# Performance work log

Measured on AMD Instinct MI355X. Metric: run time of the kernel, lower is better.

## Reference

```python
import jax, jax.numpy as jnp
import numpy as np
import math

PHI = (1.0 + math.sqrt(5.0)) / 2.0
ALPHA = 0.01
I_ROT = math.pi / 2.0
B, IN, H = 4096, 1024, 1024
GIN = IN + 4 * H  # input + 2H (h flat) + 2H (surfaced flat)


def _mag(z):
    return jnp.sqrt(z[..., 0] ** 2 + z[..., 1] ** 2 + 1e-8)


def _phase(z):
    return jnp.arctan2(z[..., 1], z[..., 0] + 1e-10)


@jax.custom_vjp
def fractal_compress(mag):
    m = jnp.maximum(mag, 1e-8)
    return m ** (2.0 / 3.0)


def _fc_fwd(mag):
    m = jnp.maximum(mag, 1e-8)
    c = m ** (2.0 / 3.0)
    return c, c / (m + 1e-6)


def _fc_bwd(ratio, g):
    return (g * jnp.minimum(ratio, 2.0),)


fractal_compress.defvjp(_fc_fwd, _fc_bwd)


def converge(z):
    mag = _mag(z)
    ph = _phase(z)
    cm = fractal_compress(mag)
    return jnp.stack([cm * jnp.cos(ph), cm * jnp.sin(ph)], axis=-1)


def resonance_gate(a, b):
    d = _phase(a) - _phase(b)
    return jnp.cos(d / 2.0) ** 2


def _uni(k, shape, fan_in):
    s = (1.0 / PHI) / math.sqrt(fan_in)
    return jax.random.uniform(k, shape, jnp.float32, -s, s)


def setup_inputs() -> dict:
    key = jax.random.key(0)
    ks = jax.random.split(key, 12)
    return {
        "x_t": jax.random.normal(ks[0], (B, IN), jnp.float32),
        "h_prev": jax.random.normal(ks[1], (B, H, 2), jnp.float32),
        "c_prev": jax.random.normal(ks[2], (B, H, 2), jnp.float32),
        "d_prev": jax.random.normal(ks[3], (B, H, 2), jnp.float32),
        "b_prev": jax.random.uniform(ks[4], (B, 1), jnp.float32),
        "Wf_w": _uni(ks[5], (H, GIN), GIN), "Wf_b": jnp.zeros((H,), jnp.float32),
        "Wi_w": _uni(ks[6], (H, GIN), GIN), "Wi_b": jnp.zeros((H,), jnp.float32),
        "Wo_w": _uni(ks[7], (H, GIN), GIN), "Wo_b": jnp.zeros((H,), jnp.float32),
        "Wc_w": _uni(ks[8], (2 * H, GIN), GIN), "Wc_b": jnp.zeros((2 * H,), jnp.float32),
        "Wr_w": _uni(ks[9], (2 * H, IN), IN), "Wr_b": jnp.zeros((2 * H,), jnp.float32),
        "theta": jnp.full((H,), I_ROT, jnp.float32),
    }


def reference(x_t, h_prev, c_prev, d_prev, b_prev,
              Wf_w, Wf_b, Wi_w, Wi_b, Wo_w, Wo_b, Wc_w, Wc_b, Wr_w, Wr_b, theta):
    batch = x_t.shape[0]
    hid = theta.shape[0]

    # boundary: real input -> complex
    x_complex = (x_t @ Wr_w.T + Wr_b).reshape(batch, hid, 2)

    # memory surfacing from the (detached) worldline
    d_read = jax.lax.stop_gradient(d_prev)
    T = resonance_gate(x_complex, d_read)                      # (B, H)
    d_mag = _mag(d_read)[..., None]                            # (B, H, 1)
    d_normed = d_read / (d_mag + 1e-8)
    d_scale = jnp.sqrt(jnp.clip(d_mag, 1e-6, 20.0))
    surfaced = d_normed * d_scale * T[..., None]               # (B, H, 2)

    combined = jnp.concatenate(
        [x_t, h_prev.reshape(batch, -1), surfaced.reshape(batch, -1)], axis=-1)

    f_raw = combined @ Wf_w.T + Wf_b
    i_raw = combined @ Wi_w.T + Wi_b
    o_raw = combined @ Wo_w.T + Wo_b

    temperature = (2.0 * b_prev + 1e-4)[..., None]             # (B, 1, 1)
    gate_stack = jnp.stack([f_raw, i_raw, o_raw], axis=-1)     # (B, H, 3)
    gw = jax.nn.softmax(gate_stack / temperature, axis=-1)
    f_t, i_t, o_t = gw[..., 0], gw[..., 1], gw[..., 2]

    g_raw = combined @ Wc_w.T + Wc_b
    g_t = jnp.stack([jnp.tanh(g_raw[:, :hid]), jnp.tanh(g_raw[:, hid:])], axis=-1)

    # convergence: released surface -> fractal-compressed -> worldline
    released = (1.0 - f_t)[..., None] * c_prev
    compressed = jnp.clip(converge(released), -10.0, 10.0)
    d_t = jax.lax.stop_gradient(d_prev) + ALPHA * compressed
    d_mag_new = _mag(d_t)[..., None]
    d_t = jnp.where(d_mag_new > 20.0, d_t * (20.0 / d_mag_new), d_t)

    # cell update + i-rotation
    c_updated = f_t[..., None] * c_prev + i_t[..., None] * g_t
    cos_t = jnp.cos(theta)[None, :, None]
    sin_t = jnp.sin(theta)[None, :, None]
    cr, ci = c_updated[..., 0:1], c_updated[..., 1:2]
    c_t = jnp.concatenate([cos_t * cr - sin_t * ci, sin_t * cr + cos_t * ci], axis=-1)

    c_squashed = jnp.stack([jnp.tanh(c_t[..., 0]), jnp.tanh(c_t[..., 1])], axis=-1)
    h_raw = o_t[..., None] * c_squashed
    G = resonance_gate(h_raw, d_t)
    h_t = G[..., None] * h_raw

    # balance update from energy split
    conv_e = (_mag(released) ** 2).sum(axis=-1, keepdims=True)
    emer_e = (_mag(h_t) ** 2).sum(axis=-1, keepdims=True)
    b_measured = conv_e / (conv_e + emer_e + 1e-8)
    b_t = 0.99 * b_prev + 0.01 * b_measured

    h_t = jnp.nan_to_num(h_t, nan=0.0)
    c_t = jnp.nan_to_num(c_t, nan=0.0)
    d_t = jnp.nan_to_num(d_t, nan=0.0)
    b_t = jnp.nan_to_num(b_t, nan=0.5)
    return (h_t, c_t, d_t, b_t)
```

## Files before the change

### kernel.cpp

```cpp
#include <hip/hip_runtime.h>
#include <math.h>

typedef unsigned short u16;
typedef unsigned int u32;
typedef u16 u16x4 __attribute__((ext_vector_type(4)));
typedef float f32x2 __attribute__((ext_vector_type(2)));
typedef float f32x4 __attribute__((ext_vector_type(4)));
typedef __bf16 bf16x8 __attribute__((ext_vector_type(8)));

#define CAPF 256

__device__ __forceinline__ u16 f2bf(float f){
  u32 u = __builtin_bit_cast(u32, f);
  u32 r = u + 0x7FFFu + ((u >> 16) & 1u);
  return (u16)(r >> 16);
}
__device__ __forceinline__ float bf2f(u16 h){
  u32 u = ((u32)h) << 16;
  return __builtin_bit_cast(float, u);
}
__device__ __forceinline__ float ftanh(float x){
  float e = __expf(2.f*x);
  return 1.f - 2.f/(e+1.f);
}

typedef __attribute__((address_space(1))) const unsigned int gas_u32;
typedef __attribute__((address_space(3))) unsigned int las_u32;
__device__ __forceinline__ void gload_lds16(const void* g, void* l){
  __builtin_amdgcn_global_load_lds((gas_u32*)g, (las_u32*)l, 16, 0, 0);
}

__global__ __launch_bounds__(256) void prep0(
    const float* __restrict__ x, const float* __restrict__ h,
    u16* __restrict__ cA, u16* __restrict__ xlo,
    const float* __restrict__ Wr, u16* __restrict__ Wr_hi, u16* __restrict__ Wr_lo,
    const float* __restrict__ bp, int* __restrict__ idx, int* __restrict__ smap,
    float* __restrict__ rawfix)
{
  const int bx = blockIdx.x, tid = threadIdx.x;
  if (bx < 12288){
    int b = bx / 3, cb = bx - b*3;
    int c0 = (cb*256 + tid)*4;
    f32x4 v;
    if (c0 < 1024) v = *(const f32x4*)(x + (size_t)b*1024 + c0);
    else           v = *(const f32x4*)(h + (size_t)b*2048 + (c0-1024));
    u16x4 hi4;
    #pragma unroll
    for (int j=0;j<4;++j) hi4[j]=f2bf(v[j]);
    *(u16x4*)(cA + (size_t)b*5120 + c0) = hi4;
    if (c0 < 1024){
      u16x4 lo4;
      #pragma unroll
      for (int j=0;j<4;++j) lo4[j]=f2bf(v[j]-bf2f(hi4[j]));
      *(u16x4*)(xlo + (size_t)b*1024 + c0) = lo4;
    }
  } else if (bx < 14336){
    int i = (bx-12288)*256 + tid;
    f32x4 v = *(const f32x4*)(Wr + (size_t)i*4);
    u16x4 oh, ol;
    #pragma unroll
    for (int j=0;j<4;++j){ u16 hh=f2bf(v[j]); oh[j]=hh; ol[j]=f2bf(v[j]-bf2f(hh)); }
    *(u16x4*)(Wr_hi + (size_t)i*4) = oh;
    *(u16x4*)(Wr_lo + (size_t)i*4) = ol;
  } else if (bx < 15104){
    int i = (bx-14336)*256 + tid;
    *(f32x4*)(rawfix + (size_t)i*4) = f32x4{0.f,0.f,0.f,0.f};
  } else {
    __shared__ int cnt;
    if (tid==0) cnt=0;
    __syncthreads();
    for (int i=tid; i<4096; i+=256){
      int p = -1;
      if (bp[i] < 0.04f){
        p = atomicAdd(&cnt,1);
        if (p < CAPF) idx[1+p]=i;
      }
      smap[i] = p;
    }
    __syncthreads();
    if (tid==0) idx[0] = min(cnt, CAPF);
  }
}

__global__ __launch_bounds__(256) void cvtW3(
    const float* __restrict__ W0, const float* __restrict__ W1, const float* __restrict__ W2,
    u16* __restrict__ out)
{
  int i = blockIdx.x*256 + threadIdx.x;
  int seg = i / 1310720;
  int w = i - seg*1310720;
  const float* src = (seg==0) ? W0 : (seg==1 ? W1 : W2);
  f32x4 v = *(const f32x4*)(src + (size_t)w*4);
  u16x4 o;
  #pragma unroll
  for (int j=0;j<4;++j) o[j]=f2bf(v[j]);
  *(u16x4*)(out + (size_t)seg*5242880 + (size_t)w*4) = o;
}

__global__ __launch_bounds__(256) void cvt_hi(const float* __restrict__ in, u16* __restrict__ out, int n4){
  int i = blockIdx.x*256 + threadIdx.x;
  if (i >= n4) return;
  f32x4 v = *(const f32x4*)(in + (size_t)i*4);
  u16x4 o;
  #pragma unroll
  for (int j=0;j<4;++j) o[j]=f2bf(v[j]);
  *(u16x4*)(out + (size_t)i*4) = o;
}

__global__ __launch_bounds__(256) void prep_surf(const float* __restrict__ xc, const float* __restrict__ dp,
                                                 const int* __restrict__ smap, float* __restrict__ Scmp,
                                                 u16* __restrict__ cA){
  int i = blockIdx.x*256 + threadIdx.x;
  int b = i >> 10, h = i & 1023;
  f32x2 z = *(const f32x2*)(xc + 2*(size_t)i);
  f32x2 d = *(const f32x2*)(dp + 2*(size_t)i);
  float zx = z[0] + 1e-10f, dx = d[0] + 1e-10f;
  float hz = sqrtf(zx*zx + z[1]*z[1]);
  float hd = sqrtf(dx*dx + d[1]*d[1]);
  float cosd = (zx*dx + z[1]*d[1]) / fmaxf(hz*hd, 1e-30f);
  float T = 0.5f + 0.5f*cosd;
  float dmag = sqrtf(d[0]*d[0] + d[1]*d[1] + 1e-8f);
  float dscale = sqrtf(fminf(fmaxf(dmag, 1e-6f), 20.0f));
  float s = T * dscale / (dmag + 1e-8f);
  float o0 = d[0]*s, o1 = d[1]*s;
  u32 pk = (u32)f2bf(o0) | ((u32)f2bf(o1) << 16);
  *(u32*)&cA[(size_t)b*5120 + 3072 + 2*h] = pk;
  int p = smap[b];
  if (p >= 0 && p < CAPF)
    *(f32x2*)(Scmp + ((size_t)p*1024 + h)*2) = f32x2{o0, o1};
}

#define STG2B(U, BW) do{ int uc_ = min((U), NH-1); \
    const u16* sa_ = Ah + aS + (size_t)uc_*32; \
    u16* da_ = sA + (BW)*4096 + w4*512; \
    gload_lds16(sa_, da_); \
    gload_lds16(sa_ + (size_t)64*lda, da_ + 2048); \
    const u16* sb_ = Bh + bS + (size_t)uc_*32; \
    u16* db_ = sB + (BW)*BUFB + w4*512; \
    _Pragma("unroll") for (int j_=0;j_<BNC;++j_) \
      gload_lds16(sb_ + (size_t)(j_*64)*ldb, db_ + j_*2048); \
  }while(0)

template<int NF, int BUFS, bool OUTBF, int NB>
__global__ __launch_bounds__(256) void gemm2b(
    const u16* __restrict__ Ah, int lda,
    const u16* __restrict__ Bh, int ldb,
    const float* __restrict__ bias0, const float* __restrict__ bias1, const float* __restrict__ bias2,
    float* __restrict__ Cf, u16* __restrict__ Cb, int ldc, int K)
{
  constexpr int BN   = NF*32;
  constexpr int BNC  = BN/64;
  constexpr int LPH  = 2 + BNC;
  constexpr int VN   = (BUFS-2)*LPH;
  constexpr int BUFB = BN*32;
  __shared__ u16 sA[BUFS*4096];
  __shared__ u16 sB[BUFS*BUFB];

  const int tid = threadIdx.x, lane = tid&63, w4 = tid>>6;
  const int wm = w4>>1, wn = w4&1;
  const int l16 = lane&15;

  const int gx = gridDim.x, nwg = gx*gridDim.y;
  const int lin = blockIdx.y*gx + blockIdx.x;
  const int sw = (lin&7)*(nwg>>3) + (lin>>3);
  const int m0 = (sw / gx)*128, n0 = (sw % gx)*BN;

  const int rowS = tid>>2;
  const int ksS  = (tid&3) ^ ((tid>>3)&3);
  const size_t aS = (size_t)(m0 + rowS)*lda + ksS*8;
  const size_t bS = (size_t)(n0 + rowS)*ldb + ksS*8;

  const int slot  = (lane>>4) ^ ((l16>>1)&3);
  const int abase = (wm*64 + l16)*32 + slot*8;
  const int bbase = (wn*(NF*16) + l16)*32 + slot*8;

  f32x4 acc[4][NF];
  #pragma unroll
  for (int a=0;a<4;++a)
    #pragma unroll
    for (int b=0;b<NF;++b) acc[a][b] = f32x4{0.f,0.f,0.f,0.f};

  const int NH = K>>5;

  #pragma unroll
  for (int u=0; u<BUFS-1; ++u){ STG2B(u, u); }
  asm volatile("s_waitcnt vmcnt(%0)" :: "i"(VN) : "memory");
  asm volatile("" ::: "memory");
  __builtin_amdgcn_s_barrier();

  int bufR = 0;
  for (int t=0; t<NH; ++t){
    int bufW = bufR + (BUFS-1); if (bufW >= BUFS) bufW -= BUFS;
    const u16* pa_ = sA + bufR*4096;
    const u16* pb_ = sB + bufR*BUFB;
    bf16x8 af0 = *(const bf16x8*)(pa_ + abase + 0*512);
    bf16x8 af1 = *(const bf16x8*)(pa_ + abase + 1*512);
    bf16x8 af2 = *(const bf16x8*)(pa_ + abase + 2*512);
    bf16x8 af3 = *(const bf16x8*)(pa_ + abase + 3*512);
    bf16x8 bfr[NF];
    #pragma unroll
    for (int n=0;n<NF;++n) bfr[n] = *(const bf16x8*)(pb_ + bbase + n*512);
    STG2B(t+BUFS-1, bufW);
    asm volatile("" ::: "memory");
    __builtin_amdgcn_s_barrier();
    __builtin_amdgcn_s_setprio(1);
    #pragma unroll
    for (int n=0;n<NF;++n){
      acc[0][n] = __builtin_amdgcn_mfma_f32_16x16x32_bf16(af0, bfr[n], acc[0][n],0,0,0);
      acc[1][n] = __builtin_amdgcn_mfma_f32_16x16x32_bf16(af1, bfr[n], acc[1][n],0,0,0);
      acc[2][n] = __builtin_amdgcn_mfma_f32_16x16x32_bf16(af2, bfr[n], acc[2][n],0,0,0);
      acc[3][n] = __builtin_amdgcn_mfma_f32_16x16x32_bf16(af3, bfr[n], acc[3][n],0,0,0);
    }
    __builtin_amdgcn_s_setprio(0);
    asm volatile("s_waitcnt vmcnt(%0)" :: "i"(VN) : "memory");
    asm volatile("" ::: "memory");
    __builtin_amdgcn_s_barrier();
    bufR = (bufR+1==BUFS) ? 0 : bufR+1;
  }
  asm volatile("s_waitcnt vmcnt(0)" ::: "memory");

  #pragma unroll
  for (int mf=0; mf<4; ++mf){
    int grow = m0 + wm*64 + mf*16 + (lane>>4)*4;
    #pragma unroll
    for (int n=0; n<NF; ++n){
      int gcol = n0 + wn*(NF*16) + n*16 + l16;
      float bb;
      if constexpr(NB==3) bb = (gcol<1024) ? bias0[gcol] : ((gcol<2048) ? bias1[gcol-1024] : bias2[gcol-2048]);
      else bb = bias0[gcol];
      #pragma unroll
      for (int r2=0;r2<4;++r2){
        float v = acc[mf][n][r2] + bb;
        if constexpr(OUTBF) Cb[(size_t)(grow+r2)*ldc + gcol] = f2bf(v);
        else                Cf[(size_t)(grow+r2)*ldc + gcol] = v;
      }
    }
  }
}

#define LDA8(BUF,H,MH,J) (*(const bf16x8*)(sAc + ((BUF)*2+(H))*16384 + abase + (MH)*4096 + (J)*1024))
#define LDB8(BUF,H,N)    (*(const bf16x8*)(sBc + ((BUF)*2+(H))*16384 + bbase + (N)*1024))
#define STG_A8(BUF,H,TT) { const u16* s_ = Ah + aS + (size_t)(TT)*64 + (H)*32; \
    gload_lds16(s_, dA + ((BUF)*2+(H))*8192); \
    gload_lds16(s_ + aS2, dA + ((BUF)*2+(H))*8192 + 4096); }
#define STG_B8(BUF,H,TT) { const u16* s_ = Bh + bS + (size_t)(TT)*64 + (H)*32; \
    gload_lds16(s_, dB + ((BUF)*2+(H))*8192); \
    gload_lds16(s_ + bS2, dB + ((BUF)*2+(H))*8192 + 4096); }
#define PH8(BUF,H,MH,RB,STG,DOW) do{ \
    bf16x8 af0 = LDA8(BUF,H,MH,0), af1 = LDA8(BUF,H,MH,1), af2 = LDA8(BUF,H,MH,2), af3 = LDA8(BUF,H,MH,3); \
    if (RB){ _Pragma("unroll") for(int n_=0;n_<NR;++n_) bfr[n_] = LDB8(BUF,H,n_); } \
    STG; \
    asm volatile("" ::: "memory"); \
    __builtin_amdgcn_s_barrier(); \
    __builtin_amdgcn_s_setprio(1); \
    _Pragma("unroll") for(int n_=0;n_<NR;++n_){ \
      acc[(MH)*4+0][n_] = __builtin_amdgcn_mfma_f32_16x16x32_bf16(af0, bfr[n_], acc[(MH)*4+0][n_],0,0,0); \
      acc[(MH)*4+1][n_] = __builtin_amdgcn_mfma_f32_16x16x32_bf16(af1, bfr[n_], acc[(MH)*4+1][n_],0,0,0); \
      acc[(MH)*4+2][n_] = __builtin_amdgcn_mfma_f32_16x16x32_bf16(af2, bfr[n_], acc[(MH)*4+2][n_],0,0,0); \
      acc[(MH)*4+3][n_] = __builtin_amdgcn_mfma_f32_16x16x32_bf16(af3, bfr[n_], acc[(MH)*4+3][n_],0,0,0); } \
    __builtin_amdgcn_s_setprio(0); \
    if (DOW) { asm volatile("s_waitcnt vmcnt(%0)" :: "i"(VN) : "memory"); } \
    asm volatile("" ::: "memory"); \
    __builtin_amdgcn_s_barrier(); \
  }while(0)

template<int NR, bool OUTBF, int NB>
__global__ __launch_bounds__(512) void gemm8p(
    const u16* __restrict__ Ah, int lda,
    const u16* __restrict__ Bh, int ldb,
    const float* __restrict__ bias0, const float* __restrict__ bias1, const float* __restrict__ bias2,
    float* __restrict__ Cf, u16* __restrict__ Cb, int ldc, int K)
{
  constexpr int BN   = NR*64;
  constexpr int VN   = 8;
  __shared__ u16 sA[4*8192];
  __shared__ u16 sB[4*8192];
  const char* sAc = (const char*)sA;
  const char* sBc = (const char*)sB;

  const int tid = threadIdx.x, lane = tid&63, w8 = tid>>6;
  const int wr = w8>>2, wc = w8&3;
  const int l16 = lane&15;

  const int gx = gridDim.x, nwg = gx*gridDim.y;
  const int lin = blockIdx.y*gx + blockIdx.x;
  const int sw = (lin&7)*(nwg>>3) + (lin>>3);
  const int m0 = (sw / gx)*256, n0 = (sw % gx)*BN;

  const int rowS  = tid>>2;
  const int ksS   = (tid&3) ^ ((tid>>3)&3);
  const size_t aS = (size_t)(m0 + rowS)*lda + ksS*8;
  const size_t aS2= (size_t)128*lda;
  const size_t bS = (size_t)(n0 + rowS)*ldb + ksS*8;
  const size_t bS2= (size_t)128*ldb;
  u16* dA = sA + w8*512;
  u16* dB = sB + w8*512;

  const int aslot = (lane>>4) ^ ((l16>>1)&3);
  const int abase = (wr*128 + l16)*64 + aslot*16;
  const int bbase = (wc*(NR*16) + l16)*64 + aslot*16;

  f32x4 acc[8][NR];
  #pragma unroll
  for (int a=0;a<8;++a)
    #pragma unroll
    for (int b=0;b<NR;++b) acc[a][b] = f32x4{0.f,0.f,0.f,0.f};
  bf16x8 bfr[NR];

  const int NT = K>>6, NITER = K>>7;

  STG_A8(0,0,0) STG_B8(0,0,0) STG_A8(0,1,0) STG_B8(0,1,0) STG_A8(1,0,1) STG_B8(1,0,1)
  asm volatile("s_waitcnt vmcnt(%0)" :: "i"(VN) : "memory");
  asm volatile("" ::: "memory");
  __builtin_amdgcn_s_barrier();

  for (int i=0; i<NITER; ++i){
    const int t1 = 2*i+1;
    const int ta = min(2*i+2, NT-1);
    const int tb = min(2*i+3, NT-1);
    PH8(0,0,0,true,  STG_A8(1,1,t1), false);
    PH8(0,0,1,false, STG_B8(1,1,t1), true);
    PH8(0,1,0,true,  STG_A8(0,0,ta), false);
    PH8(0,1,1,false, STG_B8(0,0,ta), true);
    PH8(1,0,0,true,  STG_A8(0,1,ta), false);
    PH8(1,0,1,false, STG_B8(0,1,ta), true);
    PH8(1,1,0,true,  STG_A8(1,0,tb), false);
    PH8(1,1,1,false, STG_B8(1,0,tb), true);
  }
  asm volatile("s_waitcnt vmcnt(0)" ::: "memory");

  #pragma unroll
  for (int mf=0; mf<8; ++mf){
    int grow = m0 + wr*128 + mf*16 + (lane>>4)*4;
    #pragma unroll
    for (int n=0; n<NR; ++n){
      int gcol = n0 + wc*(NR*16) + n*16 + l16;
      float bb;
      if constexpr(NB==3) bb = (gcol<1024) ? bias0[gcol] : ((gcol<2048) ? bias1[gcol-1024] : bias2[gcol-2048]);
      else bb = bias0[gcol];
      #pragma unroll
      for (int r2=0;r2<4;++r2){
        float v = acc[mf][n][r2] + bb;
        if constexpr(OUTBF) Cb[(size_t)(grow+r2)*ldc + gcol] = f2bf(v);
        else                Cf[(size_t)(grow+r2)*ldc + gcol] = v;
      }
    }
  }
}

#define STG128(USRC, BW) do{ int u_=(USRC)<NT?(USRC):NT-1; \
    { const u16* s_=Ah+aS+(size_t)u_*32; gload_lds16(s_, sA+(BW)*4096+ldsb); } \
    { const u16* s_=Bh+bS+(size_t)u_*32; gload_lds16(s_, sB+(BW)*8192+ldsb); \
      gload_lds16(s_+bS2, sB+(BW)*8192+4096+ldsb); } \
    if constexpr(SPLIT){ \
      const u16* s2_=Al+aSl+(size_t)u_*32; gload_lds16(s2_, sAl+(BW)*4096+ldsb); \
      const u16* s3_=Bl+bS+(size_t)u_*32;  gload_lds16(s3_, sBl+(BW)*8192+ldsb); \
      gload_lds16(s3_+bS2, sBl+(BW)*8192+4096+ldsb); } \
  }while(0)

template<bool SPLIT, bool OUTBF, int BUFS>
__global__ __launch_bounds__(512) void gemm128(
    const u16* __restrict__ Ah, int lda,
    const u16* __restrict__ Al, int ldal,
    const u16* __restrict__ Bh, int ldb,
    const u16* __restrict__ Bl,
    const float* __restrict__ bias0,
    float* __restrict__ Cf, u16* __restrict__ Cb, int ldc, int K)
{
  constexpr int LPS = SPLIT ? 6 : 3;
  constexpr int VN  = (BUFS-2)*LPS;
  constexpr int PRE = BUFS-1;
  __shared__ u16 sA [BUFS*4096];
  __shared__ u16 sB [BUFS*8192];
  __shared__ u16 sAl[SPLIT?BUFS*4096:8];
  __shared__ u16 sBl[SPLIT?BUFS*8192:8];

  const int tid=threadIdx.x, lane=tid&63, w8=tid>>6;
  const int wr=w8>>2, wc=w8&3, l16=lane&15;

  const int gx=gridDim.x, nwg=gx*gridDim.y;
  const int lin=blockIdx.y*gx+blockIdx.x;
  const int sw=(lin&7)*(nwg>>3)+(lin>>3);
  const int m0=(sw/gx)*128, n0=(sw%gx)*256;

  const int rowS=tid>>2;
  const int ksS=(tid&3)^((tid>>3)&3);
  const size_t aS =(size_t)(m0+rowS)*lda  + ksS*8;
  const size_t aSl=(size_t)(m0+rowS)*(size_t)ldal + ksS*8;
  const size_t bS =(size_t)(n0+rowS)*ldb  + ksS*8;
  const size_t bS2=(size_t)128*ldb;
  const int ldsb = w8*512;

  const int aslot=(lane>>4)^((l16>>1)&3);
  const int abase=(wr*64+l16)*64 + aslot*16;
  const int bbase=(wc*64+l16)*64 + aslot*16;

  f32x4 acc[4][4];
  #pragma unroll
  for (int a=0;a<4;++a)
    #pragma unroll
    for (int b=0;b<4;++b) acc[a][b] = f32x4{0.f,0.f,0.f,0.f};

  const int NT = K>>5;

  #pragma unroll
  for (int u=0; u<PRE; ++u){ STG128(u,u); }
  asm volatile("s_waitcnt vmcnt(%0)" :: "i"(VN) : "memory");
  asm volatile("" ::: "memory");
  __builtin_amdgcn_s_barrier();

  int bufR = 0;
  for (int t=0; t<NT; ++t){
    int bufW = (bufR==0) ? BUFS-1 : bufR-1;
    const char* sAc=(const char*)sA  + bufR*8192;
    const char* sBc=(const char*)sB  + bufR*16384;
    const char* sAlc=(const char*)sAl + bufR*8192;
    const char* sBlc=(const char*)sBl + bufR*16384;
    bf16x8 af[4], bf[4], afl[4], bfl[4];
    #pragma unroll
    for (int f=0; f<4; ++f){
      af[f] = *(const bf16x8*)(sAc + abase + f*1024);
      bf[f] = *(const bf16x8*)(sBc + bbase + f*1024);
      if constexpr(SPLIT){
        afl[f] = *(const bf16x8*)(sAlc + abase + f*1024);
        bfl[f] = *(const bf16x8*)(sBlc + bbase + f*1024);
      }
    }
    STG128(t+PRE, bufW);
    asm volatile("" ::: "memory");
    __builtin_amdgcn_s_barrier();
    __builtin_amdgcn_s_setprio(1);
    #pragma unroll
    for (int mf=0; mf<4; ++mf){
      #pragma unroll
      for (int nf=0; nf<4; ++nf){
        acc[mf][nf] = __builtin_amdgcn_mfma_f32_16x16x32_bf16(af[mf], bf[nf], acc[mf][nf],0,0,0);
        if constexpr(SPLIT){
          acc[mf][nf] = __builtin_amdgcn_mfma_f32_16x16x32_bf16(afl[mf], bf[nf],  acc[mf][nf],0,0,0);
          acc[mf][nf] = __builtin_amdgcn_mfma_f32_16x16x32_bf16(af[mf],  bfl[nf], acc[mf][nf],0,0,0);
        }
      }
    }
    __builtin_amdgcn_s_setprio(0);
    asm volatile("s_waitcnt vmcnt(%0)" :: "i"(VN) : "memory");
    asm volatile("" ::: "memory");
    __builtin_amdgcn_s_barrier();
    bufR = (bufR+1==BUFS) ? 0 : bufR+1;
  }
  asm volatile("s_waitcnt vmcnt(0)" ::: "memory");

  #pragma unroll
  for (int mf=0; mf<4; ++mf){
    int grow = m0 + wr*64 + mf*16 + (lane>>4)*4;
    #pragma unroll
    for (int nf=0; nf<4; ++nf){
      int gcol = n0 + wc*64 + nf*16 + l16;
      float bb = bias0[gcol];
      #pragma unroll
      for (int r2=0;r2<4;++r2){
        float v = acc[mf][nf][r2] + bb;
        if constexpr(OUTBF) Cb[(size_t)(grow+r2)*ldc + gcol] = f2bf(v);
        else                Cf[(size_t)(grow+r2)*ldc + gcol] = v;
      }
    }
  }
}

#define LSTR 40
#define FIX_KC 16
#define FIX_KLEN 320
__global__ __launch_bounds__(256) void gemm_fix_sk(
    const float* __restrict__ Xs, const float* __restrict__ Hs,
    const float* __restrict__ Scmp, const int* __restrict__ smap,
    const float* __restrict__ W0, const float* __restrict__ W1, const float* __restrict__ W2,
    const int* __restrict__ cr, float* __restrict__ Cfix)
{
  const int count = cr[0];
  const int m0 = blockIdx.y * 128;
  if (m0 >= count) return;
  const int* rows = cr + 1;
  const int kbeg = blockIdx.z * FIX_KLEN;
  const int kend = kbeg + FIX_KLEN;

  __shared__ u16 sAh[128*LSTR];
  __shared__ u16 sAl[128*LSTR];
  __shared__ u16 sBh[128*LSTR];
  __shared__ u16 sBl[128*LSTR];

  const int tid = threadIdx.x;
  const int n0 = blockIdx.x * 128;
  int seg = n0 >> 10;
  const float* W = (seg==0) ? W0 : (seg==1 ? W1 : W2);
  int nw = n0 & 1023;

  const int wave = tid >> 6, lane = tid & 63;
  const int wm = wave >> 1, wn = wave & 1;
  const int l16 = lane & 15, lk8 = (lane >> 4) * 8;

  f32x4 acc[4][4];
  #pragma unroll
  for (int a=0;a<4;++a)
    #pragma unroll
    for (int b=0;b<4;++b) acc[a][b] = f32x4{0.f,0.f,0.f,0.f};

  for (int k0 = kbeg; k0 < kend; k0 += 32){
    #pragma unroll
    for (int i=0;i<4;++i){
      int flat = tid + i*256;
      int r  = flat >> 3;
      int c4 = flat & 7;
      int kk = k0 + c4*4;
      int mi = min(m0 + r, count-1);
      int mrow = rows[mi];
      const float* srcA;
      if (kk < 1024)      srcA = Xs + (size_t)mrow*1024 + kk;
      else if (kk < 3072) srcA = Hs + (size_t)mrow*2048 + (kk - 1024);
      else                srcA = Scmp + (size_t)smap[mrow]*2048 + (kk - 3072);
      f32x4 va = *(const f32x4*)srcA;
      f32x4 vb = *(const f32x4*)(W + (size_t)(nw + r)*5120 + kk);
      u16x4 ah, bh, al, bl;
      #pragma unroll
      for (int j=0;j<4;++j){
        u16 hA = f2bf(va[j]); ah[j] = hA; al[j] = f2bf(va[j] - bf2f(hA));
        u16 hB = f2bf(vb[j]); bh[j] = hB; bl[j] = f2bf(vb[j] - bf2f(hB));
      }
      int o = r*LSTR + c4*4;
      *(u16x4*)&sAh[o] = ah;
      *(u16x4*)&sBh[o] = bh;
      *(u16x4*)&sAl[o] = al;
      *(u16x4*)&sBl[o] = bl;
    }
    __syncthreads();
    bf16x8 fah[4], fbh[4], fal[4], fbl[4];
    #pragma unroll
    for (int f=0; f<4; ++f){
      int ra  = (wm*64 + f*16 + l16)*LSTR + lk8;
      int rb2 = (wn*64 + f*16 + l16)*LSTR + lk8;
      fah[f] = *(const bf16x8*)&sAh[ra];
      fbh[f] = *(const bf16x8*)&sBh[rb2];
      fal[f] = *(const bf16x8*)&sAl[ra];
      fbl[f] = *(const bf16x8*)&sBl[rb2];
    }
    #pragma unroll
    for (int fm=0; fm<4; ++fm){
      #pragma unroll
      for (int fn=0; fn<4; ++fn){
        acc[fm][fn] = __builtin_amdgcn_mfma_f32_16x16x32_bf16(fah[fm], fbh[fn], acc[fm][fn], 0,0,0);
        acc[fm][fn] = __builtin_amdgcn_mfma_f32_16x16x32_bf16(fal[fm], fbh[fn], acc[fm][fn], 0,0,0);
        acc[fm][fn] = __builtin_amdgcn_mfma_f32_16x16x32_bf16(fah[fm], fbl[fn], acc[fm][fn], 0,0,0);
      }
    }
    __syncthreads();
  }

  #pragma unroll
  for (int fm=0; fm<4; ++fm){
    int trow = wm*64 + fm*16 + (lane>>4)*4;
    #pragma unroll
    for (int fn=0; fn<4; ++fn){
      int lcol = wn*64 + fn*16 + l16;
      #pragma unroll
      for (int r2=0;r2<4;++r2){
        int mi = m0 + trow + r2;
        if (mi < count){
          atomicAdd(&Cfix[(size_t)mi*3072 + (n0 + lcol)], acc[fm][fn][r2]);
        }
      }
    }
  }
}

__global__ __launch_bounds__(256) void epilogue(
    const float* __restrict__ rawfio, const u16* __restrict__ rawg,
    const float* __restrict__ rawfix, const int* __restrict__ smap, const int* __restrict__ cr,
    const float* __restrict__ bf0, const float* __restrict__ bf1, const float* __restrict__ bf2,
    const float* __restrict__ c_prev, const float* __restrict__ d_prev,
    const float* __restrict__ b_prev, const float* __restrict__ theta,
    float* __restrict__ out)
{
  const int b = blockIdx.x;
  const int tid = threadIdx.x;
  float* Hout = out;
  float* Cout = out + (size_t)8388608;
  float* Dout = out + (size_t)16777216;
  float* Bout = out + (size_t)25165824;
  const float bp = b_prev[b];
  const float inv_t = 1.0f / (2.0f*bp + 1e-4f);
  float conv_acc = 0.f, emer_acc = 0.f;
  const size_t rb3 = (size_t)b*3072;
  const size_t rg = (size_t)b*2048;
  const int p = smap[b];
  const bool fx = (p >= 0 && p < cr[0]);
  const size_t rfx = (size_t)p*3072;

  #pragma unroll
  for (int j=0;j<4;++j){
    int h = tid + j*256;
    float fr, ir, og;
    if (fx){
      fr = rawfix[rfx + h]        + bf0[h];
      ir = rawfix[rfx + 1024 + h] + bf1[h];
      og = rawfix[rfx + 2048 + h] + bf2[h];
    } else {
      fr = rawfio[rb3 + h];
      ir = rawfio[rb3 + 1024 + h];
      og = rawfio[rb3 + 2048 + h];
    }
    float g0 = bf2f(rawg[rg + h]);
    float g1 = bf2f(rawg[rg + 1024 + h]);

    float mx = fmaxf(fr, fmaxf(ir, og));
    float ef = __expf((fr-mx)*inv_t);
    float ei = __expf((ir-mx)*inv_t);
    float eo = __expf((og-mx)*inv_t);
    float inv_s = 1.0f/(ef+ei+eo);
    float ft = ef*inv_s, it = ei*inv_s, ot = eo*inv_s;

    f32x2 cp = *(const f32x2*)(c_prev + 2*((size_t)b*1024 + h));
    f32x2 dp = *(const f32x2*)(d_prev + 2*((size_t)b*1024 + h));

    float r0 = (1.f-ft)*cp[0], r1 = (1.f-ft)*cp[1];
    float rm2 = r0*r0 + r1*r1;
    conv_acc += rm2 + 1e-8f;
    float rmag = sqrtf(rm2 + 1e-8f);
    float cm = __expf(0.66666667f * __logf(rmag));
    float rx = r0 + 1e-10f;
    float hr = fmaxf(sqrtf(rx*rx + r1*r1), 1e-30f);
    float invhr = cm / hr;
    float comp0 = fminf(fmaxf(rx*invhr, -10.f), 10.f);
    float comp1 = fminf(fmaxf(r1*invhr, -10.f), 10.f);

    float d0 = dp[0] + 0.01f*comp0;
    float d1 = dp[1] + 0.01f*comp1;
    float dmn = sqrtf(d0*d0 + d1*d1 + 1e-8f);
    if (dmn > 20.f){ float sc = 20.f/dmn; d0*=sc; d1*=sc; }

    float gt0 = ftanh(g0), gt1 = ftanh(g1);
    float cu0 = ft*cp[0] + it*gt0;
    float cu1 = ft*cp[1] + it*gt1;
    float th = theta[h];
    float sth, cth;
    __sincosf(th, &sth, &cth);
    float c0 = cth*cu0 - sth*cu1;
    float c1 = sth*cu0 + cth*cu1;
    float cs0 = ftanh(c0), cs1 = ftanh(c1);
    float hr0 = ot*cs0, hr1 = ot*cs1;

    float hx = hr0 + 1e-10f, dx = d0 + 1e-10f;
    float hh = sqrtf(hx*hx + hr1*hr1);
    float hd = sqrtf(dx*dx + d1*d1);
    float cosd = (hx*dx + hr1*d1) / fmaxf(hh*hd, 1e-30f);
    float G = 0.5f + 0.5f*cosd;
    float h0 = G*hr0, h1 = G*hr1;
    emer_acc += h0*h0 + h1*h1 + 1e-8f;

    h0 = (h0==h0)?h0:0.f;  h1 = (h1==h1)?h1:0.f;
    c0 = (c0==c0)?c0:0.f;  c1 = (c1==c1)?c1:0.f;
    d0 = (d0==d0)?d0:0.f;  d1 = (d1==d1)?d1:0.f;

    size_t oi = 2*((size_t)b*1024 + h);
    *(f32x2*)(Hout+oi) = f32x2{h0,h1};
    *(f32x2*)(Cout+oi) = f32x2{c0,c1};
    *(f32x2*)(Dout+oi) = f32x2{d0,d1};
  }

  #pragma unroll
  for (int off=32; off; off>>=1){
    conv_acc += __shfl_down(conv_acc, off);
    emer_acc += __shfl_down(emer_acc, off);
  }
  __shared__ float sred[8];
  int wv = tid>>6, ln = tid&63;
  if (ln==0){ sred[wv]=conv_acc; sred[4+wv]=emer_acc; }
  __syncthreads();
  if (tid==0){
    float cv = sred[0]+sred[1]+sred[2]+sred[3];
    float em = sred[4]+sred[5]+sred[6]+sred[7];
    float bm = cv/(cv+em+1e-8f);
    float bt = 0.99f*bp + 0.01f*bm;
    bt = (bt==bt)?bt:0.5f;
    Bout[b] = bt;
  }
}

extern "C" void kernel_launch(void* const* d_in, const int* in_sizes, int n_in,
                              void* d_out, int out_size, void* d_ws, size_t ws_size,
                              hipStream_t stream)
{
  const float* x_t    = (const float*)d_in[0];
  const float* h_prev = (const float*)d_in[1];
  const float* c_prev = (const float*)d_in[2];
  const float* d_prev = (const float*)d_in[3];
  const float* b_prev = (const float*)d_in[4];
  const float* Wf_w   = (const float*)d_in[5];
  const float* Wf_b   = (const float*)d_in[6];
  const float* Wi_w   = (const float*)d_in[7];
  const float* Wi_b   = (const float*)d_in[8];
  const float* Wo_w   = (const float*)d_in[9];
  const float* Wo_b   = (const float*)d_in[10];
  const float* Wc_w   = (const float*)d_in[11];
  const float* Wc_b   = (const float*)d_in[12];
  const float* Wr_w   = (const float*)d_in[13];
  const float* Wr_b   = (const float*)d_in[14];
  const float* theta  = (const float*)d_in[15];

  char* W = (char*)d_ws;
  float* rawfio = (float*)W;
  float* xc     = (float*)W;
  u16*   Wr_hi  = (u16*)(W + 50331648);
  u16*   Wr_lo  = (u16*)(W + 50331648 + 4194304);
  u16*   x_lo   = (u16*)(W + 50331648 + 8388608);
  u16*   raw_g  = (u16*)(W + 50331648);
  u16*   cA     = (u16*)(W + 67108864);
  u16*   WD     = (u16*)(W + 109051904);
  int*   idx    = (int*)(W + 140509184);
  int*   smap   = (int*)(W + 140509184 + 16388);
  float* Scmp   = (float*)(W + 140546048);
  float* rawfix = (float*)(W + 140546048 + (size_t)CAPF*2048*4);

  dim3 blk(256);

  prep0<<<15105, blk, 0, stream>>>(x_t, h_prev, cA, x_lo, Wr_w, Wr_hi, Wr_lo,
                                   b_prev, idx, smap, rawfix);
  gemm128<true,false,3><<<dim3(8,32), dim3(512), 0, stream>>>(
      cA, 5120, x_lo, 1024, Wr_hi, 1024, Wr_lo,
      Wr_b, xc, nullptr, 2048, 1024);
  prep_surf<<<16384, blk, 0, stream>>>(xc, d_prev, smap, Scmp, cA);
  gemm_fix_sk<<<dim3(24,8,FIX_KC), blk, 0, stream>>>(
      x_t, h_prev, Scmp, smap, Wf_w, Wi_w, Wo_w, idx, rawfix);
  cvtW3<<<15360, blk, 0, stream>>>(Wf_w, Wi_w, Wo_w, WD);
  gemm2b<6,3,false,3><<<dim3(16,32), blk, 0, stream>>>(
      cA, 5120, WD, 5120, Wf_b, Wi_b, Wo_b, rawfio, nullptr, 3072, 5120);
  cvt_hi<<<10240, blk, 0, stream>>>(Wc_w, WD, 2621440);
  gemm2b<4,3,true,1><<<dim3(16,32), blk, 0, stream>>>(
      cA, 5120, WD, 5120, Wc_b, nullptr, nullptr, nullptr, raw_g, 2048, 5120);
  epilogue<<<4096, blk, 0, stream>>>(rawfio, raw_g, rawfix, smap, idx,
                                     Wf_b, Wi_b, Wo_b,
                                     c_prev, d_prev, b_prev, theta, (float*)d_out);
}
```

Baseline: 498.2 us.

## Fuse surfacing prep into Wr GEMM epilogue and switch gate GEMM to 8-wave bf16 output

```diff
diff --git a/kernel.cpp b/kernel.cpp
--- a/kernel.cpp
+++ b/kernel.cpp
@@ -105,29 +105,6 @@
   #pragma unroll
   for (int j=0;j<4;++j) o[j]=f2bf(v[j]);
   *(u16x4*)(out + (size_t)i*4) = o;
-}
-
-__global__ __launch_bounds__(256) void prep_surf(const float* __restrict__ xc, const float* __restrict__ dp,
-                                                 const int* __restrict__ smap, float* __restrict__ Scmp,
-                                                 u16* __restrict__ cA){
-  int i = blockIdx.x*256 + threadIdx.x;
-  int b = i >> 10, h = i & 1023;
-  f32x2 z = *(const f32x2*)(xc + 2*(size_t)i);
-  f32x2 d = *(const f32x2*)(dp + 2*(size_t)i);
-  float zx = z[0] + 1e-10f, dx = d[0] + 1e-10f;
-  float hz = sqrtf(zx*zx + z[1]*z[1]);
-  float hd = sqrtf(dx*dx + d[1]*d[1]);
-  float cosd = (zx*dx + z[1]*d[1]) / fmaxf(hz*hd, 1e-30f);
-  float T = 0.5f + 0.5f*cosd;
-  float dmag = sqrtf(d[0]*d[0] + d[1]*d[1] + 1e-8f);
-  float dscale = sqrtf(fminf(fmaxf(dmag, 1e-6f), 20.0f));
-  float s = T * dscale / (dmag + 1e-8f);
-  float o0 = d[0]*s, o1 = d[1]*s;
-  u32 pk = (u32)f2bf(o0) | ((u32)f2bf(o1) << 16);
-  *(u32*)&cA[(size_t)b*5120 + 3072 + 2*h] = pk;
-  int p = smap[b];
-  if (p >= 0 && p < CAPF)
-    *(f32x2*)(Scmp + ((size_t)p*1024 + h)*2) = f32x2{o0, o1};
 }
 
 #define STG2B(U, BW) do{ int uc_ = min((U), NH-1); \
@@ -271,7 +248,6 @@
     const float* __restrict__ bias0, const float* __restrict__ bias1, const float* __restrict__ bias2,
     float* __restrict__ Cf, u16* __restrict__ Cb, int ldc, int K)
 {
-  constexpr int BN   = NR*64;
   constexpr int VN   = 8;
   __shared__ u16 sA[4*8192];
   __shared__ u16 sB[4*8192];
@@ -285,7 +261,7 @@
   const int gx = gridDim.x, nwg = gx*gridDim.y;
   const int lin = blockIdx.y*gx + blockIdx.x;
   const int sw = (lin&7)*(nwg>>3) + (lin>>3);
-  const int m0 = (sw / gx)*256, n0 = (sw % gx)*BN;
+  const int m0 = (sw / gx)*256, n0 = (sw % gx)*(NR*64);
 
   const int rowS  = tid>>2;
   const int ksS   = (tid&3) ^ ((tid>>3)&3);
@@ -365,7 +341,9 @@
     const u16* __restrict__ Bh, int ldb,
     const u16* __restrict__ Bl,
     const float* __restrict__ bias0,
-    float* __restrict__ Cf, u16* __restrict__ Cb, int ldc, int K)
+    float* __restrict__ Cf, u16* __restrict__ Cb, int ldc, int K,
+    const float* __restrict__ dprev, const int* __restrict__ smap,
+    float* __restrict__ Scmp, u16* __restrict__ cAs)
 {
   constexpr int LPS = SPLIT ? 6 : 3;
   constexpr int VN  = (BUFS-2)*LPS;
@@ -459,8 +437,32 @@
       #pragma unroll
       for (int r2=0;r2<4;++r2){
         float v = acc[mf][nf][r2] + bb;
-        if constexpr(OUTBF) Cb[(size_t)(grow+r2)*ldc + gcol] = f2bf(v);
-        else                Cf[(size_t)(grow+r2)*ldc + gcol] = v;
+        if constexpr(SPLIT){
+          float w = __shfl_xor(v, 1);
+          if ((l16 & 1) == 0){
+            int row = grow + r2;
+            float zre = v + 1e-10f, zim = w;
+            f32x2 d = *(const f32x2*)(dprev + (size_t)row*2048 + gcol);
+            float dx = d[0] + 1e-10f;
+            float hz = sqrtf(zre*zre + zim*zim);
+            float hd = sqrtf(dx*dx + d[1]*d[1]);
+            float cosd = (zre*dx + zim*d[1]) / fmaxf(hz*hd, 1e-30f);
+            float T = 0.5f + 0.5f*cosd;
+            float dmag = sqrtf(d[0]*d[0] + d[1]*d[1] + 1e-8f);
+            float dscale = sqrtf(fminf(fmaxf(dmag, 1e-6f), 20.0f));
+            float s = T * dscale / (dmag + 1e-8f);
+            float o0 = d[0]*s, o1 = d[1]*s;
+            u32 pk = (u32)f2bf(o0) | ((u32)f2bf(o1) << 16);
+            *(u32*)&cAs[(size_t)row*5120 + 3072 + gcol] = pk;
+            int p = smap[row];
+            if (p >= 0 && p < CAPF)
+              *(f32x2*)(Scmp + (size_t)p*2048 + gcol) = f32x2{o0, o1};
+          }
+        } else if constexpr(OUTBF) {
+          Cb[(size_t)(grow+r2)*ldc + gcol] = f2bf(v);
+        } else {
+          Cf[(size_t)(grow+r2)*ldc + gcol] = v;
+        }
       }
     }
   }
@@ -571,7 +573,7 @@
 }
 
 __global__ __launch_bounds__(256) void epilogue(
-    const float* __restrict__ rawfio, const u16* __restrict__ rawg,
+    const u16* __restrict__ rawfio, const u16* __restrict__ rawg,
     const float* __restrict__ rawfix, const int* __restrict__ smap, const int* __restrict__ cr,
     const float* __restrict__ bf0, const float* __restrict__ bf1, const float* __restrict__ bf2,
     const float* __restrict__ c_prev, const float* __restrict__ d_prev,
@@ -602,9 +604,9 @@
       ir = rawfix[rfx + 1024 + h] + bf1[h];
       og = rawfix[rfx + 2048 + h] + bf2[h];
     } else {
-      fr = rawfio[rb3 + h];
-      ir = rawfio[rb3 + 1024 + h];
-      og = rawfio[rb3 + 2048 + h];
+      fr = bf2f(rawfio[rb3 + h]);
+      ir = bf2f(rawfio[rb3 + 1024 + h]);
+      og = bf2f(rawfio[rb3 + 2048 + h]);
     }
     float g0 = bf2f(rawg[rg + h]);
     float g1 = bf2f(rawg[rg + 1024 + h]);
@@ -705,8 +707,7 @@
   const float* theta  = (const float*)d_in[15];
 
   char* W = (char*)d_ws;
-  float* rawfio = (float*)W;
-  float* xc     = (float*)W;
+  u16*   rawfio = (u16*)W;
   u16*   Wr_hi  = (u16*)(W + 50331648);
   u16*   Wr_lo  = (u16*)(W + 50331648 + 4194304);
   u16*   x_lo   = (u16*)(W + 50331648 + 8388608);
@@ -724,13 +725,13 @@
                                    b_prev, idx, smap, rawfix);
   gemm128<true,false,3><<<dim3(8,32), dim3(512), 0, stream>>>(
       cA, 5120, x_lo, 1024, Wr_hi, 1024, Wr_lo,
-      Wr_b, xc, nullptr, 2048, 1024);
-  prep_surf<<<16384, blk, 0, stream>>>(xc, d_prev, smap, Scmp, cA);
+      Wr_b, nullptr, nullptr, 0, 1024,
+      d_prev, smap, Scmp, cA);
   gemm_fix_sk<<<dim3(24,8,FIX_KC), blk, 0, stream>>>(
       x_t, h_prev, Scmp, smap, Wf_w, Wi_w, Wo_w, idx, rawfix);
   cvtW3<<<15360, blk, 0, stream>>>(Wf_w, Wi_w, Wo_w, WD);
-  gemm2b<6,3,false,3><<<dim3(16,32), blk, 0, stream>>>(
-      cA, 5120, WD, 5120, Wf_b, Wi_b, Wo_b, rawfio, nullptr, 3072, 5120);
+  gemm8p<3,true,3><<<dim3(16,16), dim3(512), 0, stream>>>(
+      cA, 5120, WD, 5120, Wf_b, Wi_b, Wo_b, nullptr, rawfio, 3072, 5120);
   cvt_hi<<<10240, blk, 0, stream>>>(Wc_w, WD, 2621440);
   gemm2b<4,3,true,1><<<dim3(16,32), blk, 0, stream>>>(
       cA, 5120, WD, 5120, Wc_b, nullptr, nullptr, nullptr, raw_g, 2048, 5120);
```

After: 502.9 us. Within noise of the previous version (+0.9%).
